# Performance work log

Measured on AMD Instinct MI355X. Metric: run time of the kernel, lower is better.

Reference implementation:

```python
import jax, jax.numpy as jnp
import numpy as np

NEG_BIG = 1e20


def setup_inputs() -> dict:
    key = jax.random.key(0)
    k1, k2, k3 = jax.random.split(key, 3)
    B, Tenc, Tdec, D = 8, 2048, 512, 1024
    enc = jax.random.normal(k1, (B, Tenc, D), dtype=jnp.float32)
    dec = jax.random.normal(k2, (B, Tdec, D), dtype=jnp.float32)
    enc_mask = jax.random.randint(k3, (B, Tenc), 0, 2, dtype=jnp.int32)
    # guarantee at least one valid position per row to keep softmax well-defined
    enc_mask = enc_mask.at[:, 0].set(1)
    return {"enc": enc, "enc_mask": enc_mask, "dec": dec}


def reference(enc, enc_mask, dec):
    # dropout=0 and identity transforms -> enc_trans = enc, dec_trans = dec
    mask = enc_mask.astype(enc.dtype)  # (B, Tenc)
    # raw scores: sum_d dec[b,u,d] * enc[b,t,d] -> (B, Tenc, Tdec)
    raw = jnp.einsum('btd,bud->btu', enc, dec)
    raw = raw - (1.0 - mask)[:, :, None] * NEG_BIG
    scores = jax.nn.softmax(raw, axis=1)  # softmax over Tenc
    # context: sum_t scores[b,t,u] * enc[b,t,d] -> (B, Tdec, D)
    context = jnp.einsum('btu,btd->bud', scores, enc)
    return context, scores
```

## Files before the change

### kernel.cpp

```cpp
#include <hip/hip_runtime.h>
#include <math.h>

#define BATCH 8
#define TENC 2048
#define TDEC 512
#define DIM 1024
#define NEG_BIG 1e20f

typedef __attribute__((ext_vector_type(8))) short short8;
typedef __attribute__((ext_vector_type(4))) float f32x4;
typedef unsigned short ushort_t;

__device__ __forceinline__ unsigned int bf16rn(float x) {
    unsigned int u = __float_as_uint(x);
    return (u + 0x7FFFu + ((u >> 16) & 1u)) >> 16;
}
__device__ __forceinline__ float bf16f(unsigned int b) {
    return __uint_as_float(b << 16);
}
__device__ __forceinline__ void split2(float x, unsigned int& h, unsigned int& l) {
    h = bf16rn(x);
    l = bf16rn(x - bf16f(h));
}

#define GLOAD16(g, l)                                                        \
    __builtin_amdgcn_global_load_lds(                                        \
        (const __attribute__((address_space(1))) unsigned int*)(g),          \
        (__attribute__((address_space(3))) unsigned int*)(l), 16, 0, 0)

__device__ __forceinline__ size_t tiled_off(int row, int k, int ntK) {
    return ((size_t)(row >> 4) * ntK + (k >> 5)) * 512
         + ((k >> 3) & 3) * 128 + (row & 15) * 8;
}


__global__ __launch_bounds__(256) void prep_enc(
    const float* __restrict__ enc, ushort_t* __restrict__ encH,
    ushort_t* __restrict__ encL, ushort_t* __restrict__ encT)
{
    __shared__ ushort_t T[64][72];

    const int b  = blockIdx.z;
    const int t0 = blockIdx.y * 64;
    const int d0 = blockIdx.x * 64;
    const int tid = threadIdx.x;

    const float* E = enc + (size_t)b * TENC * DIM;
    const size_t bofs1 = (size_t)b * TENC * DIM;
    const size_t bofs2 = (size_t)b * DIM * TENC;

    const int ltr = tid >> 2;

#pragma unroll
    for (int it = 0; it < 2; ++it) {
        const int c  = (tid & 3) + it * 4;
        const int gt = t0 + ltr;
        const int gd = d0 + c * 8;
        float4 x0 = *(const float4*)&E[(size_t)gt * DIM + gd];
        float4 x1 = *(const float4*)&E[(size_t)gt * DIM + gd + 4];
        float xs[8] = {x0.x, x0.y, x0.z, x0.w, x1.x, x1.y, x1.z, x1.w};
        unsigned int h[8], l[8];
        short8 hv, lv;
#pragma unroll
        for (int j = 0; j < 8; ++j) {
            split2(xs[j], h[j], l[j]);
            hv[j] = (short)h[j];
            lv[j] = (short)l[j];
        }
        const size_t off = bofs1 + tiled_off(gt, gd, DIM / 32);
        *(short8*)&encH[off] = hv;
        *(short8*)&encL[off] = lv;
#pragma unroll
        for (int j = 0; j < 8; ++j) T[c * 8 + j][ltr] = (ushort_t)h[j];
    }
    __syncthreads();

    const int dr = tid >> 2;
#pragma unroll
    for (int it = 0; it < 2; ++it) {
        const int tc = (tid & 3) + it * 4;
        const int gd = d0 + dr;
        const int gt = t0 + tc * 8;
        short8 v = *(const short8*)&T[dr][tc * 8];
        *(short8*)&encT[bofs2 + tiled_off(gd, gt, TENC / 32)] = v;
    }
}

__global__ __launch_bounds__(256) void prep_dec(
    const float* __restrict__ dec, ushort_t* __restrict__ decH,
    ushort_t* __restrict__ decL)
{
    const int b  = blockIdx.z;
    const int u0 = blockIdx.y * 64;
    const int d0 = blockIdx.x * 64;
    const int tid = threadIdx.x;

    const float* D = dec + (size_t)b * TDEC * DIM;
    const size_t bofs = (size_t)b * TDEC * DIM;

    const int lur = tid >> 2;

#pragma unroll
    for (int it = 0; it < 2; ++it) {
        const int c  = (tid & 3) + it * 4;
        const int gu = u0 + lur;
        const int gd = d0 + c * 8;
        float4 x0 = *(const float4*)&D[(size_t)gu * DIM + gd];
        float4 x1 = *(const float4*)&D[(size_t)gu * DIM + gd + 4];
        float xs[8] = {x0.x, x0.y, x0.z, x0.w, x1.x, x1.y, x1.z, x1.w};
        short8 hv, lv;
#pragma unroll
        for (int j = 0; j < 8; ++j) {
            unsigned int h, l;
            split2(xs[j], h, l);
            hv[j] = (short)h;
            lv[j] = (short)l;
        }
        const size_t off = bofs + tiled_off(gu, gd, DIM / 32);
        *(short8*)&decH[off] = hv;
        *(short8*)&decL[off] = lv;
    }
}

__global__ __launch_bounds__(256) void gemm1_lds(
    const ushort_t* __restrict__ encH, const ushort_t* __restrict__ encL,
    const ushort_t* __restrict__ decH, const ushort_t* __restrict__ decL,
    const int* __restrict__ mask, float* __restrict__ raw,
    float* __restrict__ pm, float* __restrict__ ps)
{
    __shared__ __align__(16) ushort_t Ah[128 * 32];
    __shared__ __align__(16) ushort_t Al[128 * 32];
    __shared__ __align__(16) ushort_t Bh[128 * 32];
    __shared__ __align__(16) ushort_t Bl[128 * 32];
    __shared__ float smx[4][68];
    __shared__ float ssx[4][68];

    const int b  = blockIdx.z;
    const int m0 = blockIdx.y * 128;
    const int n0 = blockIdx.x * 128;
    const int tid = threadIdx.x;

    const int lane = tid & 63;
    const int w    = tid >> 6;
    const int wm   = (w & 1) * 64;
    const int wn   = (w >> 1) * 64;
    const int lr   = lane & 15;
    const int q    = lane >> 4;
    const int l8   = lane * 8;

    const int fa = wm * 32 + q * 128 + lr * 8;
    const int fb = wn * 32 + q * 128 + lr * 8;

    const ushort_t* AH = encH + (size_t)b * TENC * DIM;
    const ushort_t* AL = encL + (size_t)b * TENC * DIM;
    const ushort_t* BH = decH + (size_t)b * TDEC * DIM;
    const ushort_t* BL = decL + (size_t)b * TDEC * DIM;
    float* C = raw + (size_t)b * TENC * TDEC;

    f32x4 acc[4][4] = {};

    for (int k0 = 0; k0 < DIM; k0 += 32) {
        __syncthreads();
#pragma unroll
        for (int q2 = 0; q2 < 2; ++q2) {
            const int rg = w * 2 + q2;
            const size_t tA = ((size_t)((m0 >> 4) + rg) * (DIM / 32) + (k0 >> 5)) * 512 + l8;
            const size_t tB = ((size_t)((n0 >> 4) + rg) * (DIM / 32) + (k0 >> 5)) * 512 + l8;
            GLOAD16(AH + tA, &Ah[rg * 512]);
            GLOAD16(AL + tA, &Al[rg * 512]);
            GLOAD16(BH + tB, &Bh[rg * 512]);
            GLOAD16(BL + tB, &Bl[rg * 512]);
        }
        __syncthreads();

        short8 ah[4], al[4], bh[4], bl[4];
#pragma unroll
        for (int i = 0; i < 4; ++i) {
            ah[i] = *(const short8*)&Ah[fa + i * 512];
            al[i] = *(const short8*)&Al[fa + i * 512];
            bh[i] = *(const short8*)&Bh[fb + i * 512];
            bl[i] = *(const short8*)&Bl[fb + i * 512];
        }
#pragma unroll
        for (int i = 0; i < 4; ++i)
#pragma unroll
            for (int j = 0; j < 4; ++j) {
                acc[i][j] = __builtin_amdgcn_mfma_f32_16x16x32_bf16(ah[i], bh[j], acc[i][j], 0, 0, 0);
                acc[i][j] = __builtin_amdgcn_mfma_f32_16x16x32_bf16(ah[i], bl[j], acc[i][j], 0, 0, 0);
                acc[i][j] = __builtin_amdgcn_mfma_f32_16x16x32_bf16(al[i], bh[j], acc[i][j], 0, 0, 0);
            }
    }

    float mkv[4][4];
#pragma unroll
    for (int i = 0; i < 4; ++i)
#pragma unroll
        for (int rr = 0; rr < 4; ++rr) {
            const int t = m0 + wm + i * 16 + q * 4 + rr;
            mkv[i][rr] = (mask[b * TENC + t] == 0) ? NEG_BIG : 0.0f;
        }

    float cm[4] = {-INFINITY, -INFINITY, -INFINITY, -INFINITY};
    float cs[4] = {0.f, 0.f, 0.f, 0.f};
#pragma unroll
    for (int i = 0; i < 4; ++i)
#pragma unroll
        for (int rr = 0; rr < 4; ++rr) {
            const int t = m0 + wm + i * 16 + q * 4 + rr;
#pragma unroll
            for (int j = 0; j < 4; ++j) {
                const int u = n0 + wn + j * 16 + lr;
                const float v = acc[i][j][rr] - mkv[i][rr];
                C[(size_t)t * TDEC + u] = v;
                cm[j] = fmaxf(cm[j], v);
            }
        }
#pragma unroll
    for (int i = 0; i < 4; ++i)
#pragma unroll
        for (int rr = 0; rr < 4; ++rr)
#pragma unroll
            for (int j = 0; j < 4; ++j)
                cs[j] += __expf(acc[i][j][rr] - mkv[i][rr] - cm[j]);

#pragma unroll
    for (int j = 0; j < 4; ++j) {
#pragma unroll
        for (int d = 16; d < 64; d <<= 1) {
            float om = __shfl_xor(cm[j], d, 64);
            float os = __shfl_xor(cs[j], d, 64);
            float mn = fmaxf(cm[j], om);
            cs[j] = cs[j] * __expf(cm[j] - mn) + os * __expf(om - mn);
            cm[j] = mn;
        }
    }

    if (q == 0) {
#pragma unroll
        for (int j = 0; j < 4; ++j) {
            smx[w][j * 16 + lr] = cm[j];
            ssx[w][j * 16 + lr] = cs[j];
        }
    }
    __syncthreads();
    if (tid < 128) {
        const int col = tid;
        const int wp  = (col >> 6) * 2;
        const int ci  = col & 63;
        const float m1 = smx[wp][ci],     s1 = ssx[wp][ci];
        const float m2 = smx[wp + 1][ci], s2 = ssx[wp + 1][ci];
        const float M = fmaxf(m1, m2);
        const float S = s1 * __expf(m1 - M) + s2 * __expf(m2 - M);
        const int idx = b * TDEC + n0 + col;
        const int tb  = m0 >> 7;
        pm[(size_t)tb * (BATCH * TDEC) + idx] = M;
        ps[(size_t)tb * (BATCH * TDEC) + idx] = S;
    }
}

__global__ __launch_bounds__(256) void colstat2(
    const float* __restrict__ pm, const float* __restrict__ ps,
    float* __restrict__ colM, float* __restrict__ colI)
{
    const int idx = blockIdx.x * 256 + threadIdx.x;
    float M = -INFINITY;
#pragma unroll
    for (int z = 0; z < 16; ++z)
        M = fmaxf(M, pm[(size_t)z * (BATCH * TDEC) + idx]);
    float s = 0.0f;
#pragma unroll
    for (int z = 0; z < 16; ++z)
        s += ps[(size_t)z * (BATCH * TDEC) + idx] *
             __expf(pm[(size_t)z * (BATCH * TDEC) + idx] - M);
    colM[idx] = M;
    colI[idx] = 1.0f / s;
}

__global__ __launch_bounds__(256) void norm_kernel(
    float* __restrict__ S, const float* __restrict__ colM,
    const float* __restrict__ colI, ushort_t* __restrict__ scoresT)
{
    __shared__ ushort_t T[64][72];

    const int b  = blockIdx.z;
    const int t0 = blockIdx.x * 64;
    const int u0 = blockIdx.y * 64;
    const int tid = threadIdx.x;

    const int tr  = tid >> 4;
    const int ucl = (tid & 15) * 4;

    float4 M4 = *(const float4*)&colM[b * TDEC + u0 + ucl];
    float4 I4 = *(const float4*)&colI[b * TDEC + u0 + ucl];

    float* base = S + (size_t)b * TENC * TDEC;

#pragma unroll
    for (int i = 0; i < 4; ++i) {
        const int t = t0 + tr + 16 * i;
        float4 x = *(const float4*)&base[(size_t)t * TDEC + u0 + ucl];
        float4 p;
        p.x = __expf(x.x - M4.x) * I4.x;
        p.y = __expf(x.y - M4.y) * I4.y;
        p.z = __expf(x.z - M4.z) * I4.z;
        p.w = __expf(x.w - M4.w) * I4.w;
        *(float4*)&base[(size_t)t * TDEC + u0 + ucl] = p;
        const int tloc = tr + 16 * i;
        T[ucl + 0][tloc] = (ushort_t)bf16rn(p.x);
        T[ucl + 1][tloc] = (ushort_t)bf16rn(p.y);
        T[ucl + 2][tloc] = (ushort_t)bf16rn(p.z);
        T[ucl + 3][tloc] = (ushort_t)bf16rn(p.w);
    }
    __syncthreads();

    const size_t bofs = (size_t)b * TDEC * TENC;
    const int ur = tid >> 2;
#pragma unroll
    for (int it = 0; it < 2; ++it) {
        const int tc = (tid & 3) + it * 4;
        const int gu = u0 + ur;
        const int gt = t0 + tc * 8;
        short8 v = *(const short8*)&T[ur][tc * 8];
        *(short8*)&scoresT[bofs + tiled_off(gu, gt, TENC / 32)] = v;
    }
}

__global__ __launch_bounds__(256) void gemm2_lds(
    const ushort_t* __restrict__ scoresT, const ushort_t* __restrict__ encT,
    float* __restrict__ p0, float* __restrict__ p1)
{
    __shared__ __align__(16) ushort_t Ah[128 * 32];
    __shared__ __align__(16) ushort_t Bh[128 * 32];

    const int b  = blockIdx.z >> 1;
    const int ks = blockIdx.z & 1;
    const int m0 = blockIdx.y * 128;
    const int n0 = blockIdx.x * 128;
    const int tid = threadIdx.x;

    const int lane = tid & 63;
    const int w    = tid >> 6;
    const int wm   = (w & 1) * 64;
    const int wn   = (w >> 1) * 64;
    const int lr   = lane & 15;
    const int q    = lane >> 4;
    const int l8   = lane * 8;

    const int fa = wm * 32 + q * 128 + lr * 8;
    const int fb = wn * 32 + q * 128 + lr * 8;

    const ushort_t* A = scoresT + (size_t)b * TDEC * TENC;
    const ushort_t* B = encT    + (size_t)b * DIM * TENC;
    float* P = (ks ? p1 : p0) + (size_t)b * TDEC * DIM;

    const int kbeg = ks * (TENC / 2);
    const int kend = kbeg + TENC / 2;

    f32x4 acc[4][4] = {};

    for (int k0 = kbeg; k0 < kend; k0 += 32) {
        __syncthreads();
#pragma unroll
        for (int q2 = 0; q2 < 2; ++q2) {
            const int rg = w * 2 + q2;
            const size_t tA = ((size_t)((m0 >> 4) + rg) * (TENC / 32) + (k0 >> 5)) * 512 + l8;
            const size_t tB = ((size_t)((n0 >> 4) + rg) * (TENC / 32) + (k0 >> 5)) * 512 + l8;
            GLOAD16(A + tA, &Ah[rg * 512]);
            GLOAD16(B + tB, &Bh[rg * 512]);
        }
        __syncthreads();

        short8 ah[4], bh[4];
#pragma unroll
        for (int i = 0; i < 4; ++i) {
            ah[i] = *(const short8*)&Ah[fa + i * 512];
            bh[i] = *(const short8*)&Bh[fb + i * 512];
        }
#pragma unroll
        for (int i = 0; i < 4; ++i)
#pragma unroll
            for (int j = 0; j < 4; ++j)
                acc[i][j] = __builtin_amdgcn_mfma_f32_16x16x32_bf16(ah[i], bh[j], acc[i][j], 0, 0, 0);
    }

#pragma unroll
    for (int i = 0; i < 4; ++i)
#pragma unroll
        for (int rr = 0; rr < 4; ++rr) {
            const int u = m0 + wm + i * 16 + q * 4 + rr;
#pragma unroll
            for (int j = 0; j < 4; ++j) {
                const int d = n0 + wn + j * 16 + lr;
                P[(size_t)u * DIM + d] = acc[i][j][rr];
            }
        }
}

__global__ __launch_bounds__(256) void reduce_ctx(
    const float* __restrict__ p0, const float* __restrict__ p1,
    float* __restrict__ ctx)
{
    const size_t i4 = ((size_t)blockIdx.x * 256 + threadIdx.x) * 4;
    float4 a = *(const float4*)(p0 + i4);
    float4 b = *(const float4*)(p1 + i4);
    float4 o;
    o.x = a.x + b.x; o.y = a.y + b.y; o.z = a.z + b.z; o.w = a.w + b.w;
    *(float4*)(ctx + i4) = o;
}


__device__ __forceinline__ void store8(ushort_t* ph, ushort_t* pl,
                                       float4 x0, float4 x1) {
    float xs[8] = {x0.x, x0.y, x0.z, x0.w, x1.x, x1.y, x1.z, x1.w};
    short8 hv, lv;
#pragma unroll
    for (int i = 0; i < 8; ++i) {
        unsigned int h, l;
        split2(xs[i], h, l);
        hv[i] = (short)h;
        lv[i] = (short)l;
    }
    *(short8*)ph = hv;
    *(short8*)pl = lv;
}

__device__ __forceinline__ void wr4(ushort_t* ph, ushort_t* pl, const float* x) {
    unsigned int h[4], l[4];
#pragma unroll
    for (int i = 0; i < 4; ++i) split2(x[i], h[i], l[i]);
    *(uint2*)ph = make_uint2(h[0] | (h[1] << 16), h[2] | (h[3] << 16));
    *(uint2*)pl = make_uint2(l[0] | (l[1] << 16), l[2] | (l[3] << 16));
}

__device__ __forceinline__ short8 frag8B(const ushort_t* p) {
    union { short8 v; uint2 u[2]; } f;
    f.u[0] = *(const uint2*)p;
    f.u[1] = *(const uint2*)(p + 4);
    return f.v;
}

__global__ __launch_bounds__(256) void gemm1_mfma(
    const float* __restrict__ enc, const float* __restrict__ dec,
    const int* __restrict__ mask, float* __restrict__ raw)
{
    __shared__ __align__(16) ushort_t Ah[128 * 32];
    __shared__ __align__(16) ushort_t Al[128 * 32];
    __shared__ __align__(16) ushort_t Bh[128 * 32];
    __shared__ __align__(16) ushort_t Bl[128 * 32];

    const int b  = blockIdx.z;
    const int m0 = blockIdx.y * 128;
    const int n0 = blockIdx.x * 128;
    const int tid = threadIdx.x;

    const float* A  = enc + (size_t)b * TENC * DIM;
    const float* Bg = dec + (size_t)b * TDEC * DIM;
    float*       C  = raw + (size_t)b * TENC * TDEC;

    const int lane = tid & 63;
    const int wv   = tid >> 6;
    const int wm   = (wv & 1) * 64;
    const int wn   = (wv >> 1) * 64;
    const int lr   = lane & 15;
    const int q    = lane >> 4;

    const int r0 = tid >> 2;
    const int c8 = (tid & 3) * 8;

    f32x4 acc[4][4] = {};

    for (int k0 = 0; k0 < DIM; k0 += 32) {
        const float* pa0 = A  + (size_t)(m0 + r0) * DIM + k0 + c8;
        const float* pa1 = A  + (size_t)(m0 + r0 + 64) * DIM + k0 + c8;
        const float* pb0 = Bg + (size_t)(n0 + r0) * DIM + k0 + c8;
        const float* pb1 = Bg + (size_t)(n0 + r0 + 64) * DIM + k0 + c8;
        float4 a0 = *(const float4*)pa0, a0b = *(const float4*)(pa0 + 4);
        float4 a1 = *(const float4*)pa1, a1b = *(const float4*)(pa1 + 4);
        float4 b0 = *(const float4*)pb0, b0b = *(const float4*)(pb0 + 4);
        float4 b1 = *(const float4*)pb1, b1b = *(const float4*)(pb1 + 4);

        __syncthreads();
        store8(&Ah[r0 * 32 + c8],        &Al[r0 * 32 + c8],        a0, a0b);
        store8(&Ah[(r0 + 64) * 32 + c8], &Al[(r0 + 64) * 32 + c8], a1, a1b);
        store8(&Bh[r0 * 32 + c8],        &Bl[r0 * 32 + c8],        b0, b0b);
        store8(&Bh[(r0 + 64) * 32 + c8], &Bl[(r0 + 64) * 32 + c8], b1, b1b);
        __syncthreads();

        short8 ah[4], al[4], bh[4], bl[4];
#pragma unroll
        for (int i = 0; i < 4; ++i) {
            ah[i] = *(const short8*)&Ah[(wm + i * 16 + lr) * 32 + q * 8];
            al[i] = *(const short8*)&Al[(wm + i * 16 + lr) * 32 + q * 8];
            bh[i] = *(const short8*)&Bh[(wn + i * 16 + lr) * 32 + q * 8];
            bl[i] = *(const short8*)&Bl[(wn + i * 16 + lr) * 32 + q * 8];
        }
#pragma unroll
        for (int i = 0; i < 4; ++i)
#pragma unroll
            for (int j = 0; j < 4; ++j) {
                acc[i][j] = __builtin_amdgcn_mfma_f32_16x16x32_bf16(ah[i], bh[j], acc[i][j], 0, 0, 0);
                acc[i][j] = __builtin_amdgcn_mfma_f32_16x16x32_bf16(ah[i], bl[j], acc[i][j], 0, 0, 0);
                acc[i][j] = __builtin_amdgcn_mfma_f32_16x16x32_bf16(al[i], bh[j], acc[i][j], 0, 0, 0);
            }
    }

#pragma unroll
    for (int i = 0; i < 4; ++i)
#pragma unroll
        for (int rr = 0; rr < 4; ++rr) {
            const int t = m0 + wm + i * 16 + q * 4 + rr;
            const float mk = (mask[b * TENC + t] == 0) ? NEG_BIG : 0.0f;
#pragma unroll
            for (int j = 0; j < 4; ++j) {
                const int u = n0 + wn + j * 16 + lr;
                C[(size_t)t * TDEC + u] = acc[i][j][rr] - mk;
            }
        }
}

__global__ __launch_bounds__(256) void softmax_kernel(float* __restrict__ S)
{
    const int b  = blockIdx.y;
    const int u0 = blockIdx.x * 16;
    const int up = threadIdx.x & 15;
    const int tg = threadIdx.x >> 4;

    float* col = S + (size_t)b * TENC * TDEC + u0;

    float m = -INFINITY, s = 0.0f;
    for (int t = tg; t < TENC; t += 16) {
        float x = col[(size_t)t * TDEC + up];
        float mn = fmaxf(m, x);
        s = s * __expf(m - mn) + __expf(x - mn);
        m = mn;
    }

    __shared__ float sm[16][17];
    __shared__ float ss[16][17];
    sm[tg][up] = m;
    ss[tg][up] = s;
    __syncthreads();

    float M = -INFINITY;
#pragma unroll
    for (int j = 0; j < 16; ++j) M = fmaxf(M, sm[j][up]);
    float sum = 0.0f;
#pragma unroll
    for (int j = 0; j < 16; ++j) sum += ss[j][up] * __expf(sm[j][up] - M);
    const float inv = 1.0f / sum;

    for (int t = tg; t < TENC; t += 16) {
        float x = col[(size_t)t * TDEC + up];
        col[(size_t)t * TDEC + up] = __expf(x - M) * inv;
    }
}

#define G2_LD 36

__global__ __launch_bounds__(256) void gemm2_mfma(
    const float* __restrict__ scores, const float* __restrict__ enc,
    float* __restrict__ context)
{
    __shared__ __align__(16) ushort_t Ah[128 * G2_LD];
    __shared__ __align__(16) ushort_t Al[128 * G2_LD];
    __shared__ __align__(16) ushort_t Bh[128 * G2_LD];
    __shared__ __align__(16) ushort_t Bl[128 * G2_LD];

    const int b  = blockIdx.z;
    const int m0 = blockIdx.y * 128;
    const int n0 = blockIdx.x * 128;
    const int tid = threadIdx.x;

    const float* S = scores + (size_t)b * TENC * TDEC;
    const float* E = enc    + (size_t)b * TENC * DIM;
    float*       C = context + (size_t)b * TDEC * DIM;

    const int lane = tid & 63;
    const int wv   = tid >> 6;
    const int wm   = (wv & 1) * 64;
    const int wn   = (wv >> 1) * 64;
    const int lr   = lane & 15;
    const int q    = lane >> 4;

    const int ul = tid & 127;
    const int th = (tid >> 7) * 16;

    f32x4 acc[4][4] = {};

    for (int k0 = 0; k0 < TENC; k0 += 32) {
        float av[16], bv[16];
#pragma unroll
        for (int i = 0; i < 4; ++i) {
            const int t = k0 + th + i * 4;
#pragma unroll
            for (int j = 0; j < 4; ++j) {
                av[i * 4 + j] = S[(size_t)(t + j) * TDEC + m0 + ul];
                bv[i * 4 + j] = E[(size_t)(t + j) * DIM + n0 + ul];
            }
        }
        __syncthreads();
#pragma unroll
        for (int i = 0; i < 4; ++i) {
            const int tt = th + i * 4;
            wr4(&Ah[ul * G2_LD + tt], &Al[ul * G2_LD + tt], &av[i * 4]);
            wr4(&Bh[ul * G2_LD + tt], &Bl[ul * G2_LD + tt], &bv[i * 4]);
        }
        __syncthreads();

        short8 ah[4], al[4], bh[4], bl[4];
#pragma unroll
        for (int i = 0; i < 4; ++i) {
            ah[i] = frag8B(&Ah[(wm + i * 16 + lr) * G2_LD + q * 8]);
            al[i] = frag8B(&Al[(wm + i * 16 + lr) * G2_LD + q * 8]);
            bh[i] = frag8B(&Bh[(wn + i * 16 + lr) * G2_LD + q * 8]);
            bl[i] = frag8B(&Bl[(wn + i * 16 + lr) * G2_LD + q * 8]);
        }
#pragma unroll
        for (int i = 0; i < 4; ++i)
#pragma unroll
            for (int j = 0; j < 4; ++j) {
                acc[i][j] = __builtin_amdgcn_mfma_f32_16x16x32_bf16(ah[i], bh[j], acc[i][j], 0, 0, 0);
                acc[i][j] = __builtin_amdgcn_mfma_f32_16x16x32_bf16(ah[i], bl[j], acc[i][j], 0, 0, 0);
                acc[i][j] = __builtin_amdgcn_mfma_f32_16x16x32_bf16(al[i], bh[j], acc[i][j], 0, 0, 0);
            }
    }

#pragma unroll
    for (int i = 0; i < 4; ++i)
#pragma unroll
        for (int rr = 0; rr < 4; ++rr) {
            const int u = m0 + wm + i * 16 + q * 4 + rr;
#pragma unroll
            for (int j = 0; j < 4; ++j) {
                const int d = n0 + wn + j * 16 + lr;
                C[(size_t)u * DIM + d] = acc[i][j][rr];
            }
        }
}

extern "C" void kernel_launch(void* const* d_in, const int* in_sizes, int n_in,
                              void* d_out, int out_size, void* d_ws, size_t ws_size,
                              hipStream_t stream)
{
    const float* enc      = (const float*)d_in[0];
    const int*   enc_mask = (const int*)  d_in[1];
    const float* dec      = (const float*)d_in[2];

    float* context = (float*)d_out;
    float* scores  = context + (size_t)BATCH * TDEC * DIM;

    const size_t OFF_ENC_H = 0;
    const size_t OFF_ENC_L = 33554432;
    const size_t OFF_DEC_H = 67108864;
    const size_t OFF_DEC_L = 75497472;
    const size_t OFF_ENC_T = 83886080;
    const size_t OFF_SCO_T = 117440512;
    const size_t OFF_PM    = OFF_SCO_T;
    const size_t OFF_PS    = OFF_SCO_T + 262144;
    const size_t OFF_COL_M = 134217728;
    const size_t OFF_COL_I = 134234112;
    const size_t WS_NEED   = 134381568;

    if (ws_size >= WS_NEED) {
        char* w = (char*)d_ws;
        ushort_t* encH    = (ushort_t*)(w + OFF_ENC_H);
        ushort_t* encL    = (ushort_t*)(w + OFF_ENC_L);
        ushort_t* decH    = (ushort_t*)(w + OFF_DEC_H);
        ushort_t* decL    = (ushort_t*)(w + OFF_DEC_L);
        ushort_t* encT    = (ushort_t*)(w + OFF_ENC_T);
        ushort_t* scoresT = (ushort_t*)(w + OFF_SCO_T);
        float*    pm      = (float*)(w + OFF_PM);
        float*    ps      = (float*)(w + OFF_PS);
        float*    colM    = (float*)(w + OFF_COL_M);
        float*    colI    = (float*)(w + OFF_COL_I);
        float*    part0   = (float*)(w + OFF_ENC_H);
        float*    part1   = (float*)(w + OFF_ENC_L);

        prep_enc<<<dim3(DIM / 64, TENC / 64, BATCH), 256, 0, stream>>>(
            enc, encH, encL, encT);
        prep_dec<<<dim3(DIM / 64, TDEC / 64, BATCH), 256, 0, stream>>>(
            dec, decH, decL);

        gemm1_lds<<<dim3(TDEC / 128, TENC / 128, BATCH), 256, 0, stream>>>(
            encH, encL, decH, decL, enc_mask, scores, pm, ps);

        colstat2<<<16, 256, 0, stream>>>(pm, ps, colM, colI);

        norm_kernel<<<dim3(TENC / 64, TDEC / 64, BATCH), 256, 0, stream>>>(
            scores, colM, colI, scoresT);

        gemm2_lds<<<dim3(DIM / 128, TDEC / 128, BATCH * 2), 256, 0, stream>>>(
            scoresT, encT, part0, part1);

        reduce_ctx<<<4096, 256, 0, stream>>>(part0, part1, context);
    } else {
        gemm1_mfma<<<dim3(TDEC / 128, TENC / 128, BATCH), 256, 0, stream>>>(
            enc, dec, enc_mask, scores);
        softmax_kernel<<<dim3(TDEC / 16, BATCH), 256, 0, stream>>>(scores);
        gemm2_mfma<<<dim3(DIM / 128, TDEC / 128, BATCH), 256, 0, stream>>>(
            scores, enc, context);
    }
}
```

Before: 240.0 us.

## Fuse prep kernels, fold column stats into norm, split gemm2 K four ways

Merges the enc and dec prep kernels into a single launch and drops the separate colstat kernel, so each norm block recomputes its 64 column max and sum terms from the partial stats. The partial stats now sit in the context output buffer as scratch. gemm2 splits K into four chunks instead of two to expose more blocks, and reduce_ctx sums four partial buffers. This removes two launches and raises gemm2 parallelism, at the cost of redundant stat recomputation in every norm block and extra partial-sum traffic.

Measured after the change: 243.3 us. About the same (+1.4%).

```diff
diff --git a/kernel.cpp b/kernel.cpp
--- a/kernel.cpp
+++ b/kernel.cpp
@@ -34,91 +34,84 @@
 }
 
 
-__global__ __launch_bounds__(256) void prep_enc(
-    const float* __restrict__ enc, ushort_t* __restrict__ encH,
-    ushort_t* __restrict__ encL, ushort_t* __restrict__ encT)
+__global__ __launch_bounds__(256) void prep_fused(
+    const float* __restrict__ enc, const float* __restrict__ dec,
+    ushort_t* __restrict__ encH, ushort_t* __restrict__ encL,
+    ushort_t* __restrict__ encT, ushort_t* __restrict__ decH,
+    ushort_t* __restrict__ decL)
 {
     __shared__ ushort_t T[64][72];
 
-    const int b  = blockIdx.z;
-    const int t0 = blockIdx.y * 64;
-    const int d0 = blockIdx.x * 64;
+    const int b   = blockIdx.z;
+    const int d0  = blockIdx.x * 64;
     const int tid = threadIdx.x;
 
-    const float* E = enc + (size_t)b * TENC * DIM;
-    const size_t bofs1 = (size_t)b * TENC * DIM;
-    const size_t bofs2 = (size_t)b * DIM * TENC;
-
-    const int ltr = tid >> 2;
-
-#pragma unroll
-    for (int it = 0; it < 2; ++it) {
-        const int c  = (tid & 3) + it * 4;
-        const int gt = t0 + ltr;
-        const int gd = d0 + c * 8;
-        float4 x0 = *(const float4*)&E[(size_t)gt * DIM + gd];
-        float4 x1 = *(const float4*)&E[(size_t)gt * DIM + gd + 4];
-        float xs[8] = {x0.x, x0.y, x0.z, x0.w, x1.x, x1.y, x1.z, x1.w};
-        unsigned int h[8], l[8];
-        short8 hv, lv;
-#pragma unroll
-        for (int j = 0; j < 8; ++j) {
-            split2(xs[j], h[j], l[j]);
-            hv[j] = (short)h[j];
-            lv[j] = (short)l[j];
-        }
-        const size_t off = bofs1 + tiled_off(gt, gd, DIM / 32);
-        *(short8*)&encH[off] = hv;
-        *(short8*)&encL[off] = lv;
-#pragma unroll
-        for (int j = 0; j < 8; ++j) T[c * 8 + j][ltr] = (ushort_t)h[j];
-    }
-    __syncthreads();
-
-    const int dr = tid >> 2;
-#pragma unroll
-    for (int it = 0; it < 2; ++it) {
-        const int tc = (tid & 3) + it * 4;
-        const int gd = d0 + dr;
-        const int gt = t0 + tc * 8;
-        short8 v = *(const short8*)&T[dr][tc * 8];
-        *(short8*)&encT[bofs2 + tiled_off(gd, gt, TENC / 32)] = v;
-    }
-}
-
-__global__ __launch_bounds__(256) void prep_dec(
-    const float* __restrict__ dec, ushort_t* __restrict__ decH,
-    ushort_t* __restrict__ decL)
-{
-    const int b  = blockIdx.z;
-    const int u0 = blockIdx.y * 64;
-    const int d0 = blockIdx.x * 64;
-    const int tid = threadIdx.x;
-
-    const float* D = dec + (size_t)b * TDEC * DIM;
-    const size_t bofs = (size_t)b * TDEC * DIM;
-
-    const int lur = tid >> 2;
-
-#pragma unroll
-    for (int it = 0; it < 2; ++it) {
-        const int c  = (tid & 3) + it * 4;
-        const int gu = u0 + lur;
-        const int gd = d0 + c * 8;
-        float4 x0 = *(const float4*)&D[(size_t)gu * DIM + gd];
-        float4 x1 = *(const float4*)&D[(size_t)gu * DIM + gd + 4];
-        float xs[8] = {x0.x, x0.y, x0.z, x0.w, x1.x, x1.y, x1.z, x1.w};
-        short8 hv, lv;
-#pragma unroll
-        for (int j = 0; j < 8; ++j) {
-            unsigned int h, l;
-            split2(xs[j], h, l);
-            hv[j] = (short)h;
-            lv[j] = (short)l;
-        }
-        const size_t off = bofs + tiled_off(gu, gd, DIM / 32);
-        *(short8*)&decH[off] = hv;
-        *(short8*)&decL[off] = lv;
+    if (blockIdx.y < 32) {
+        const int t0 = blockIdx.y * 64;
+        const float* E = enc + (size_t)b * TENC * DIM;
+        const size_t bofs1 = (size_t)b * TENC * DIM;
+        const size_t bofs2 = (size_t)b * DIM * TENC;
+
+        const int ltr = tid >> 2;
+#pragma unroll
+        for (int it = 0; it < 2; ++it) {
+            const int c  = (tid & 3) + it * 4;
+            const int gt = t0 + ltr;
+            const int gd = d0 + c * 8;
+            float4 x0 = *(const float4*)&E[(size_t)gt * DIM + gd];
+            float4 x1 = *(const float4*)&E[(size_t)gt * DIM + gd + 4];
+            float xs[8] = {x0.x, x0.y, x0.z, x0.w, x1.x, x1.y, x1.z, x1.w};
+            unsigned int h[8], l[8];
+            short8 hv, lv;
+#pragma unroll
+            for (int j = 0; j < 8; ++j) {
+                split2(xs[j], h[j], l[j]);
+                hv[j] = (short)h[j];
+                lv[j] = (short)l[j];
+            }
+            const size_t off = bofs1 + tiled_off(gt, gd, DIM / 32);
+            *(short8*)&encH[off] = hv;
+            *(short8*)&encL[off] = lv;
+#pragma unroll
+            for (int j = 0; j < 8; ++j) T[c * 8 + j][ltr] = (ushort_t)h[j];
+        }
+        __syncthreads();
+
+        const int dr = tid >> 2;
+#pragma unroll
+        for (int it = 0; it < 2; ++it) {
+            const int tc = (tid & 3) + it * 4;
+            const int gd = d0 + dr;
+            const int gt = t0 + tc * 8;
+            short8 v = *(const short8*)&T[dr][tc * 8];
+            *(short8*)&encT[bofs2 + tiled_off(gd, gt, TENC / 32)] = v;
+        }
+    } else {
+        const int u0 = (blockIdx.y - 32) * 64;
+        const float* D = dec + (size_t)b * TDEC * DIM;
+        const size_t bofs = (size_t)b * TDEC * DIM;
+
+        const int lur = tid >> 2;
+#pragma unroll
+        for (int it = 0; it < 2; ++it) {
+            const int c  = (tid & 3) + it * 4;
+            const int gu = u0 + lur;
+            const int gd = d0 + c * 8;
+            float4 x0 = *(const float4*)&D[(size_t)gu * DIM + gd];
+            float4 x1 = *(const float4*)&D[(size_t)gu * DIM + gd + 4];
+            float xs[8] = {x0.x, x0.y, x0.z, x0.w, x1.x, x1.y, x1.z, x1.w};
+            short8 hv, lv;
+#pragma unroll
+            for (int j = 0; j < 8; ++j) {
+                unsigned int h, l;
+                split2(xs[j], h, l);
+                hv[j] = (short)h;
+                lv[j] = (short)l;
+            }
+            const size_t off = bofs + tiled_off(gu, gd, DIM / 32);
+            *(short8*)&decH[off] = hv;
+            *(short8*)&decL[off] = lv;
+        }
     }
 }
 
@@ -258,40 +251,39 @@
     }
 }
 
-__global__ __launch_bounds__(256) void colstat2(
-    const float* __restrict__ pm, const float* __restrict__ ps,
-    float* __restrict__ colM, float* __restrict__ colI)
-{
-    const int idx = blockIdx.x * 256 + threadIdx.x;
-    float M = -INFINITY;
-#pragma unroll
-    for (int z = 0; z < 16; ++z)
-        M = fmaxf(M, pm[(size_t)z * (BATCH * TDEC) + idx]);
-    float s = 0.0f;
-#pragma unroll
-    for (int z = 0; z < 16; ++z)
-        s += ps[(size_t)z * (BATCH * TDEC) + idx] *
-             __expf(pm[(size_t)z * (BATCH * TDEC) + idx] - M);
-    colM[idx] = M;
-    colI[idx] = 1.0f / s;
-}
-
 __global__ __launch_bounds__(256) void norm_kernel(
-    float* __restrict__ S, const float* __restrict__ colM,
-    const float* __restrict__ colI, ushort_t* __restrict__ scoresT)
+    float* __restrict__ S, const float* __restrict__ pm,
+    const float* __restrict__ ps, ushort_t* __restrict__ scoresT)
 {
     __shared__ ushort_t T[64][72];
+    __shared__ float cMs[64], cIs[64];
 
     const int b  = blockIdx.z;
     const int t0 = blockIdx.x * 64;
     const int u0 = blockIdx.y * 64;
     const int tid = threadIdx.x;
 
+    if (tid < 64) {
+        const int idx = b * TDEC + u0 + tid;
+        float M = -INFINITY;
+#pragma unroll
+        for (int z = 0; z < 16; ++z)
+            M = fmaxf(M, pm[(size_t)z * (BATCH * TDEC) + idx]);
+        float s = 0.0f;
+#pragma unroll
+        for (int z = 0; z < 16; ++z)
+            s += ps[(size_t)z * (BATCH * TDEC) + idx] *
+                 __expf(pm[(size_t)z * (BATCH * TDEC) + idx] - M);
+        cMs[tid] = M;
+        cIs[tid] = 1.0f / s;
+    }
+    __syncthreads();
+
     const int tr  = tid >> 4;
     const int ucl = (tid & 15) * 4;
 
-    float4 M4 = *(const float4*)&colM[b * TDEC + u0 + ucl];
-    float4 I4 = *(const float4*)&colI[b * TDEC + u0 + ucl];
+    float4 M4 = *(const float4*)&cMs[ucl];
+    float4 I4 = *(const float4*)&cIs[ucl];
 
     float* base = S + (size_t)b * TENC * TDEC;
 
@@ -327,13 +319,14 @@
 
 __global__ __launch_bounds__(256) void gemm2_lds(
     const ushort_t* __restrict__ scoresT, const ushort_t* __restrict__ encT,
-    float* __restrict__ p0, float* __restrict__ p1)
+    float* __restrict__ p0, float* __restrict__ p1,
+    float* __restrict__ p2, float* __restrict__ p3)
 {
     __shared__ __align__(16) ushort_t Ah[128 * 32];
     __shared__ __align__(16) ushort_t Bh[128 * 32];
 
-    const int b  = blockIdx.z >> 1;
-    const int ks = blockIdx.z & 1;
+    const int b  = blockIdx.z >> 2;
+    const int ks = blockIdx.z & 3;
     const int m0 = blockIdx.y * 128;
     const int n0 = blockIdx.x * 128;
     const int tid = threadIdx.x;
@@ -351,10 +344,11 @@
 
     const ushort_t* A = scoresT + (size_t)b * TDEC * TENC;
     const ushort_t* B = encT    + (size_t)b * DIM * TENC;
-    float* P = (ks ? p1 : p0) + (size_t)b * TDEC * DIM;
-
-    const int kbeg = ks * (TENC / 2);
-    const int kend = kbeg + TENC / 2;
+    float* Psel = ks == 0 ? p0 : (ks == 1 ? p1 : (ks == 2 ? p2 : p3));
+    float* P = Psel + (size_t)b * TDEC * DIM;
+
+    const int kbeg = ks * (TENC / 4);
+    const int kend = kbeg + TENC / 4;
 
     f32x4 acc[4][4] = {};
 
@@ -398,13 +392,19 @@
 
 __global__ __launch_bounds__(256) void reduce_ctx(
     const float* __restrict__ p0, const float* __restrict__ p1,
+    const float* __restrict__ p2, const float* __restrict__ p3,
     float* __restrict__ ctx)
 {
     const size_t i4 = ((size_t)blockIdx.x * 256 + threadIdx.x) * 4;
     float4 a = *(const float4*)(p0 + i4);
     float4 b = *(const float4*)(p1 + i4);
+    float4 c = *(const float4*)(p2 + i4);
+    float4 d = *(const float4*)(p3 + i4);
     float4 o;
-    o.x = a.x + b.x; o.y = a.y + b.y; o.z = a.z + b.z; o.w = a.w + b.w;
+    o.x = a.x + b.x + c.x + d.x;
+    o.y = a.y + b.y + c.y + d.y;
+    o.z = a.z + b.z + c.z + d.z;
+    o.w = a.w + b.w + c.w + d.w;
     *(float4*)(ctx + i4) = o;
 }
 
@@ -655,11 +655,7 @@
     const size_t OFF_DEC_L = 75497472;
     const size_t OFF_ENC_T = 83886080;
     const size_t OFF_SCO_T = 117440512;
-    const size_t OFF_PM    = OFF_SCO_T;
-    const size_t OFF_PS    = OFF_SCO_T + 262144;
-    const size_t OFF_COL_M = 134217728;
-    const size_t OFF_COL_I = 134234112;
-    const size_t WS_NEED   = 134381568;
+    const size_t WS_NEED   = 134217728;
 
     if (ws_size >= WS_NEED) {
         char* w = (char*)d_ws;
@@ -669,30 +665,26 @@
         ushort_t* decL    = (ushort_t*)(w + OFF_DEC_L);
         ushort_t* encT    = (ushort_t*)(w + OFF_ENC_T);
         ushort_t* scoresT = (ushort_t*)(w + OFF_SCO_T);
-        float*    pm      = (float*)(w + OFF_PM);
-        float*    ps      = (float*)(w + OFF_PS);
-        float*    colM    = (float*)(w + OFF_COL_M);
-        float*    colI    = (float*)(w + OFF_COL_I);
         float*    part0   = (float*)(w + OFF_ENC_H);
-        float*    part1   = (float*)(w + OFF_ENC_L);
-
-        prep_enc<<<dim3(DIM / 64, TENC / 64, BATCH), 256, 0, stream>>>(
-            enc, encH, encL, encT);
-        prep_dec<<<dim3(DIM / 64, TDEC / 64, BATCH), 256, 0, stream>>>(
-            dec, decH, decL);
+        float*    part1   = (float*)(w + OFF_ENC_H + 16777216);
+        float*    part2   = (float*)(w + OFF_ENC_L);
+        float*    part3   = (float*)(w + OFF_ENC_L + 16777216);
+        float*    pm      = context;
+        float*    ps      = context + 65536;
+
+        prep_fused<<<dim3(DIM / 64, 40, BATCH), 256, 0, stream>>>(
+            enc, dec, encH, encL, encT, decH, decL);
 
         gemm1_lds<<<dim3(TDEC / 128, TENC / 128, BATCH), 256, 0, stream>>>(
             encH, encL, decH, decL, enc_mask, scores, pm, ps);
 
-        colstat2<<<16, 256, 0, stream>>>(pm, ps, colM, colI);
-
         norm_kernel<<<dim3(TENC / 64, TDEC / 64, BATCH), 256, 0, stream>>>(
-            scores, colM, colI, scoresT);
-
-        gemm2_lds<<<dim3(DIM / 128, TDEC / 128, BATCH * 2), 256, 0, stream>>>(
-            scoresT, encT, part0, part1);
-
-        reduce_ctx<<<4096, 256, 0, stream>>>(part0, part1, context);
+            scores, pm, ps, scoresT);
+
+        gemm2_lds<<<dim3(DIM / 128, TDEC / 128, BATCH * 4), 256, 0, stream>>>(
+            scoresT, encT, part0, part1, part2, part3);
+
+        reduce_ctx<<<4096, 256, 0, stream>>>(part0, part1, part2, part3, context);
     } else {
         gemm1_mfma<<<dim3(TDEC / 128, TENC / 128, BATCH), 256, 0, stream>>>(
             enc, dec, enc_mask, scores);
```
